# Optimization experiments

Hardware: AMD Instinct MI355X
Metric: run time of the kernel (lower is better)

## Reference

```python
import jax, jax.numpy as jnp
import numpy as np

B, T, I, H, V = 128, 80, 4096, 256, 6000
DEC_STEPS = 40


def _lstm_cell(x, h, c, Wih, Whh, b):
    # PyTorch gate order: i, f, g, o
    gates = x @ Wih.T + h @ Whh.T + b  # (B, 4H)
    i, f, g, o = jnp.split(gates, 4, axis=-1)
    c_new = jax.nn.sigmoid(f) * c + jax.nn.sigmoid(i) * jnp.tanh(g)
    h_new = jax.nn.sigmoid(o) * jnp.tanh(c_new)
    return h_new, c_new


def _lstm_scan(xs, h0, c0, Wih, Whh, b):
    # xs: (T, B, D)
    def step(carry, x):
        h, c = carry
        h, c = _lstm_cell(x, h, c, Wih, Whh, b)
        return (h, c), h
    (h, c), ys = jax.lax.scan(step, (h0, c0), xs)
    return ys, h, c


def setup_inputs() -> dict:
    key = jax.random.key(0)
    ks = jax.random.split(key, 11)
    s = 1.0 / np.sqrt(H)  # pytorch default LSTM init scale
    return {
        "x": jax.random.normal(ks[0], (B, T, I), jnp.float32),
        "W_ih1": jax.random.uniform(ks[1], (4 * H, I), jnp.float32, -s, s),
        "W_hh1": jax.random.uniform(ks[2], (4 * H, H), jnp.float32, -s, s),
        "b_ih1": jax.random.uniform(ks[3], (4 * H,), jnp.float32, -s, s),
        "b_hh1": jax.random.uniform(ks[4], (4 * H,), jnp.float32, -s, s),
        "W_ih2": jax.random.uniform(ks[5], (4 * H, H), jnp.float32, -s, s),
        "W_hh2": jax.random.uniform(ks[6], (4 * H, H), jnp.float32, -s, s),
        "b_ih2": jax.random.uniform(ks[7], (4 * H,), jnp.float32, -s, s),
        "b_ih2": jax.random.uniform(ks[7], (4 * H,), jnp.float32, -s, s),
        "b_hh2": jax.random.uniform(ks[8], (4 * H,), jnp.float32, -s, s),
        "W_out": jax.random.uniform(ks[9], (V, H), jnp.float32, -s, s),
        "b_out": jax.random.uniform(ks[10], (V,), jnp.float32, -s, s),
    }


def reference(x, W_ih1, W_hh1, b_ih1, b_hh1, W_ih2, W_hh2, b_ih2, b_hh2, W_out, b_out):
    batch = x.shape[0]
    b1 = b_ih1 + b_hh1
    b2 = b_ih2 + b_hh2
    z = jnp.zeros((batch, H), x.dtype)

    # --- Encoding: lstm1 over video features, lstm2 over lstm1 outputs ---
    xs = jnp.transpose(x, (1, 0, 2))  # (T, B, I)
    ys1, h1, c1 = _lstm_scan(xs, z, z, W_ih1, W_hh1, b1)
    _, h2, c2 = _lstm_scan(ys1, z, z, W_ih2, W_hh2, b2)

    # --- One extra lstm1 step with zero padding (as in the source) ---
    dec_pad = jnp.zeros((batch, I), x.dtype)
    h1, c1 = _lstm_cell(dec_pad, h1, c1, W_ih1, W_hh1, b1)
    y2 = jnp.zeros((batch, H), x.dtype)

    def dec_step(carry, _):
        h1, c1, h2, c2, y2 = carry
        h1, c1 = _lstm_cell(dec_pad, h1, c1, W_ih1, W_hh1, b1)
        h2, c2 = _lstm_cell(h1 + y2, h2, c2, W_ih2, W_hh2, b2)
        return (h1, c1, h2, c2, h2), h2

    _, ys = jax.lax.scan(dec_step, (h1, c1, h2, c2, y2), None, length=DEC_STEPS)  # (40, B, H)
    feats = jnp.transpose(ys, (1, 0, 2)).reshape(-1, H)  # (B*40, H)
    return feats @ W_out.T + b_out  # (B*40, V)
```

## Files before the change

### kernel.cpp

```cpp
#include <hip/hip_runtime.h>

#define NB 128
#define NT 80
#define NI 4096
#define NH 256
#define G4 1024
#define NV 6000
#define NVP 6016
#define NDEC 40

typedef unsigned short ushort_t;
typedef __attribute__((ext_vector_type(8))) short bf16x8;
typedef __attribute__((ext_vector_type(4))) float f32x4;

__device__ __forceinline__ unsigned short f2bf(float f) {
  unsigned int x = __float_as_uint(f);
  x += 0x7FFFu + ((x >> 16) & 1u);
  return (unsigned short)(x >> 16);
}
__device__ __forceinline__ ushort4 pack4(float4 v) {
  return make_ushort4(f2bf(v.x), f2bf(v.y), f2bf(v.z), f2bf(v.w));
}
__device__ __forceinline__ float ftanh(float x) {
  float xc = fminf(fmaxf(x, -12.f), 12.f);
  float e = __expf(2.f * xc);
  return (e - 1.f) * __builtin_amdgcn_rcpf(e + 1.f);
}
__device__ __forceinline__ float fsig(float x) {
  return __builtin_amdgcn_rcpf(1.f + __expf(-x));
}


__global__ __launch_bounds__(256) void k_cast_x(const float* __restrict__ x,
                                                ushort_t* __restrict__ xb) {
  const int t = blockIdx.x, b = blockIdx.y;
  const float* src = x + ((size_t)b * NT + t) * NI;
  ushort_t* dst = xb + ((size_t)t * NB + b) * NI;
#pragma unroll
  for (int s = 0; s < 4; ++s) {
    int j = s * 1024 + threadIdx.x * 4;
    float4 v = *(const float4*)(src + j);
    *(ushort4*)(dst + j) = pack4(v);
  }
}

__global__ __launch_bounds__(256) void k_cast_pad(const float* __restrict__ s,
                                                  ushort_t* __restrict__ d,
                                                  int nsrc, int ndst) {
  int i = (blockIdx.x * 256 + threadIdx.x) * 4;
  if (i >= ndst) return;
  ushort4 o;
  if (i < nsrc) {
    float4 v = *(const float4*)(s + i);
    o = pack4(v);
  } else {
    o = make_ushort4(0, 0, 0, 0);
  }
  *(ushort4*)(d + i) = o;
}

__global__ __launch_bounds__(256) void k_addw_bf(const float* __restrict__ a,
                                                 const float* __restrict__ b,
                                                 ushort_t* __restrict__ o) {
  int i = (blockIdx.x * 256 + threadIdx.x) * 4;
  float4 va = *(const float4*)(a + i);
  float4 vb = *(const float4*)(b + i);
  va.x += vb.x; va.y += vb.y; va.z += vb.z; va.w += vb.w;
  *(ushort4*)(o + i) = pack4(va);
}


#define GLDS(gp, lp)                                                     \
  __builtin_amdgcn_global_load_lds(                                      \
      (const __attribute__((address_space(1))) unsigned int*)(gp),       \
      (__attribute__((address_space(3))) unsigned int*)(lp), 16, 0, 0)

__global__ __launch_bounds__(256) void k_gemm(
    const ushort_t* __restrict__ A, const ushort_t* __restrict__ Bm,
    float* __restrict__ C, const float* __restrict__ ba,
    const float* __restrict__ bb, int Nreal, int K, int ldc, int mtiles) {
  __shared__ __align__(16) ushort_t Als[128 * 32];
  __shared__ __align__(16) ushort_t Bls[128 * 32];
  const int bid = blockIdx.x;
  const int mt = bid % mtiles, nt = bid / mtiles;
  const size_t m0 = (size_t)mt * 128, n0 = (size_t)nt * 128;
  const int tid = threadIdx.x, wave = tid >> 6, lane = tid & 63;
  const int wm = (wave & 1) * 64, wn = (wave >> 1) * 64;
  const int srow = wave * 16 + (lane >> 2), skcol = (lane & 3) * 8;
  const int fr = lane & 15, kb = (lane >> 4) * 8;

  f32x4 acc[4][4];
#pragma unroll
  for (int i = 0; i < 4; ++i)
#pragma unroll
    for (int j = 0; j < 4; ++j) acc[i][j] = (f32x4){0.f, 0.f, 0.f, 0.f};

  for (int kk = 0; kk < K; kk += 32) {
    __syncthreads();
#pragma unroll
    for (int p = 0; p < 2; ++p) {
      GLDS(A + (m0 + p * 64 + srow) * K + kk + skcol,
           &Als[(p * 64 + wave * 16) * 32]);
      GLDS(Bm + (n0 + p * 64 + srow) * K + kk + skcol,
           &Bls[(p * 64 + wave * 16) * 32]);
    }
    __syncthreads();
    bf16x8 af[4], bfr[4];
#pragma unroll
    for (int i = 0; i < 4; ++i)
      af[i] = *(const bf16x8*)&Als[(wm + i * 16 + fr) * 32 + kb];
#pragma unroll
    for (int j = 0; j < 4; ++j)
      bfr[j] = *(const bf16x8*)&Bls[(wn + j * 16 + fr) * 32 + kb];
#pragma unroll
    for (int i = 0; i < 4; ++i)
#pragma unroll
      for (int j = 0; j < 4; ++j)
        acc[i][j] = __builtin_amdgcn_mfma_f32_16x16x32_bf16(af[i], bfr[j],
                                                            acc[i][j], 0, 0, 0);
  }
  const int cr4 = (lane >> 4) * 4, ccn = lane & 15;
#pragma unroll
  for (int j = 0; j < 4; ++j) {
    int n = (int)n0 + wn + j * 16 + ccn;
    if (n < Nreal) {
      float bv = (ba ? ba[n] : 0.f) + (bb ? bb[n] : 0.f);
#pragma unroll
      for (int i = 0; i < 4; ++i) {
#pragma unroll
        for (int r = 0; r < 4; ++r) {
          size_t m = m0 + wm + i * 16 + cr4 + r;
          C[m * (size_t)ldc + n] = acc[i][j][r] + bv;
        }
      }
    }
  }
}


struct ChainArgs {
  const float* gIn0; const float* gIn1; int n0; int tStart; int tEnd;
  const ushort_t* W0; const ushort_t* Wsw; int swStep;
  const float* biasA; const float* biasB;
  ushort_t* traj0; ushort_t* traj1; int t1bmaj;
  ushort_t* hSt; float* cSt;
};

#define LOAD_WREGS(Wb)                                                        \
  _Pragma("unroll") for (int g = 0; g < 3; ++g)                               \
  _Pragma("unroll") for (int h = 0; h < 2; ++h)                               \
  _Pragma("unroll") for (int kb = 0; kb < 8; ++kb)                            \
      wr[g * 2 + h][kb] = *(const bf16x8*)((Wb) +                             \
          (size_t)(g * 256 + cbase + h * 16 + cn) * NH + kb * 32 + kgrp * 8);

#define PIN_W()                                                               \
  _Pragma("unroll") for (int g = 0; g < 6; ++g)                               \
  _Pragma("unroll") for (int kb = 0; kb < 8; ++kb)                            \
      asm volatile("" : "+a"(wr[g][kb]));

#define LOAD_WLDS(Wb)                                                         \
  _Pragma("unroll") for (int h = 0; h < 2; ++h)                               \
  _Pragma("unroll") for (int kb = 0; kb < 8; ++kb)                            \
      *(bf16x8*)&WL[wv * 8192 + h * 4096 + kb * 512 + cn * 32 + kgrp * 8] =   \
          *(const bf16x8*)((Wb) +                                             \
          (size_t)(768 + cbase + h * 16 + cn) * NH + kb * 32 + kgrp * 8);

__device__ __forceinline__ void run_chain(const ChainArgs a, int bg,
                                          ushort_t* WL,
                                          ushort_t (*hTz)[16 * 264]) {
  const int tid = threadIdx.x;
  const int wv = tid >> 6, lane = tid & 63;
  const int cn = lane & 15;
  const int kgrp = lane >> 4;
  const int cbase = wv * 32;
  const int rsel = kgrp & 1;

  bf16x8 wr[6][8];
  const ushort_t* Winit = (a.Wsw && a.tStart >= a.swStep) ? a.Wsw : a.W0;
  LOAD_WREGS(Winit);
  PIN_W();
  LOAD_WLDS(Winit);

  for (int i = tid; i < 2 * 16 * 264; i += 512) ((ushort_t*)hTz)[i] = 0;
  __syncthreads();
  float cs[8];
  if (a.tStart == 0) {
#pragma unroll
    for (int i = 0; i < 8; ++i) cs[i] = 0.f;
  } else {
    for (int i = tid; i < 8 * 256; i += 512) {
      int b = i >> 8, col = i & 255;
      hTz[0][b * 264 + col] = a.hSt[(size_t)(bg * 8 + b) * NH + col];
    }
#pragma unroll
    for (int h = 0; h < 2; ++h)
#pragma unroll
      for (int e = 0; e < 4; ++e)
        cs[h * 4 + e] =
            a.cSt[(size_t)(bg * 8 + rsel * 4 + e) * NH + cbase + h * 16 + cn];
  }
  __syncthreads();

  int cur = 0;
  for (int t = a.tStart; t < a.tEnd; ++t) {
    if (a.Wsw && t == a.swStep && t != a.tStart) {
      LOAD_WREGS(a.Wsw);
      PIN_W();
      LOAD_WLDS(a.Wsw);
      __syncthreads();
    }
    const ushort_t* hTc = &hTz[cur][0];
    ushort_t* hTn = &hTz[cur ^ 1][0];
    const float* gseg = (t < a.n0) ? a.gIn0 : a.gIn1;
    const int tt = (t < a.n0) ? t : t - a.n0;
#pragma unroll
    for (int h = 0; h < 2; ++h) {
      const int gcol = cbase + h * 16 + cn;
      float in_[4][4];
      if (gseg) {
        const float* base = gseg + (size_t)tt * (NB * G4);
#pragma unroll
        for (int g = 0; g < 4; ++g)
#pragma unroll
          for (int e = 0; e < 4; ++e)
            in_[g][e] = base[(size_t)(bg * 8 + rsel * 4 + e) * G4 + g * 256 + gcol];
      } else {
#pragma unroll
        for (int g = 0; g < 4; ++g) {
          float b = a.biasA[g * 256 + gcol] + a.biasB[g * 256 + gcol];
#pragma unroll
          for (int e = 0; e < 4; ++e) in_[g][e] = b;
        }
      }
      f32x4 acc[4];
#pragma unroll
      for (int g = 0; g < 4; ++g) acc[g] = (f32x4){0.f, 0.f, 0.f, 0.f};
#pragma unroll
      for (int kb = 0; kb < 8; ++kb) {
        bf16x8 af = *(const bf16x8*)&hTc[cn * 264 + kb * 32 + kgrp * 8];
        bf16x8 bo = *(const bf16x8*)&WL[wv * 8192 + h * 4096 + kb * 512 +
                                        cn * 32 + kgrp * 8];
        acc[0] = __builtin_amdgcn_mfma_f32_16x16x32_bf16(af, wr[0 + h][kb],
                                                         acc[0], 0, 0, 0);
        acc[1] = __builtin_amdgcn_mfma_f32_16x16x32_bf16(af, wr[2 + h][kb],
                                                         acc[1], 0, 0, 0);
        acc[2] = __builtin_amdgcn_mfma_f32_16x16x32_bf16(af, wr[4 + h][kb],
                                                         acc[2], 0, 0, 0);
        acc[3] = __builtin_amdgcn_mfma_f32_16x16x32_bf16(af, bo, acc[3], 0, 0, 0);
      }
#pragma unroll
      for (int e = 0; e < 4; ++e) {
        float a0 = acc[0][e] + in_[0][e];
        float a1 = acc[1][e] + in_[1][e];
        float a2 = acc[2][e] + in_[2][e];
        float a3 = acc[3][e] + in_[3][e];
        float ig = fsig(a0);
        float fg = fsig(a1);
        float gg = ftanh(a2);
        float og = fsig(a3);
        float cn_ = fg * cs[h * 4 + e] + ig * gg;
        cs[h * 4 + e] = cn_;
        float hn = og * ftanh(cn_);
        unsigned short hb = f2bf(hn);
        if (lane < 32) {
          const int b = (lane >> 4) * 4 + e;
          hTn[b * 264 + gcol] = hb;
          const int bglob = bg * 8 + b;
          if (t < a.n0) {
            if (a.traj0)
              a.traj0[(size_t)t * (NB * NH) + (size_t)bglob * NH + gcol] = hb;
          } else if (a.traj1) {
            size_t idx = a.t1bmaj
                ? ((size_t)bglob * NDEC + (t - a.n0)) * NH + gcol
                : (size_t)(t - a.n0) * (NB * NH) + (size_t)bglob * NH + gcol;
            a.traj1[idx] = hb;
          }
        }
      }
    }
    __syncthreads();
    cur ^= 1;
  }

  for (int i = tid; i < 8 * 256; i += 512) {
    int b = i >> 8, col = i & 255;
    a.hSt[(size_t)(bg * 8 + b) * NH + col] = hTz[cur][b * 264 + col];
  }
  if (lane < 32) {
#pragma unroll
    for (int h = 0; h < 2; ++h)
#pragma unroll
      for (int e = 0; e < 4; ++e)
        a.cSt[(size_t)(bg * 8 + (lane >> 4) * 4 + e) * NH + cbase + h * 16 + cn] =
            cs[h * 4 + e];
  }
}

__global__ __launch_bounds__(512, 1) void p_lstm16(ChainArgs a) {
  __shared__ __align__(16) ushort_t WL[8 * 8192];
  __shared__ __align__(16) ushort_t hTz[2][16 * 264];
  run_chain(a, blockIdx.x, WL, hTz);
}

__global__ __launch_bounds__(512, 1) void p_dual(ChainArgs a, ChainArgs b) {
  __shared__ __align__(16) ushort_t WL[8 * 8192];
  __shared__ __align__(16) ushort_t hTz[2][16 * 264];
  if (blockIdx.x < 16)
    run_chain(a, blockIdx.x, WL, hTz);
  else
    run_chain(b, blockIdx.x - 16, WL, hTz);
}


extern "C" void kernel_launch(void* const* d_in, const int* in_sizes, int n_in,
                              void* d_out, int out_size, void* d_ws,
                              size_t ws_size, hipStream_t stream) {
  const float* x = (const float*)d_in[0];
  const float* Wih1 = (const float*)d_in[1];
  const float* Whh1 = (const float*)d_in[2];
  const float* bih1 = (const float*)d_in[3];
  const float* bhh1 = (const float*)d_in[4];
  const float* Wih2 = (const float*)d_in[5];
  const float* Whh2 = (const float*)d_in[6];
  const float* bih2 = (const float*)d_in[7];
  const float* bhh2 = (const float*)d_in[8];
  const float* Wout = (const float*)d_in[9];
  const float* bout = (const float*)d_in[10];
  char* ws = (char*)d_ws;

  ushort_t* x_bf   = (ushort_t*)(ws + 0);
  float*    G2buf  = (float*)(ws + 0);
  float*    G3buf  = (float*)(ws + 41943040);
  float*    Gbuf   = (float*)(ws + 83886080);
  ushort_t* Wih1b  = (ushort_t*)(ws + 125829120);
  ushort_t* h1St   = (ushort_t*)(ws + 125829120);
  float*    c1St   = (float*)(ws + 125894656);
  ushort_t* h2St   = (ushort_t*)(ws + 126025728);
  float*    c2St   = (float*)(ws + 126091264);
  ushort_t* Wih2b  = (ushort_t*)(ws + 134217728);
  ushort_t* Woutb  = (ushort_t*)(ws + 134742016);
  ushort_t* Whh1b  = (ushort_t*)(ws + 137822208);
  ushort_t* Whh2b  = (ushort_t*)(ws + 138346496);
  ushort_t* ys1    = (ushort_t*)(ws + 138870784);
  ushort_t* H1dec  = (ushort_t*)(ws + 144113664);
  ushort_t* feats  = (ushort_t*)(ws + 146800640);
  ushort_t* Wsumb  = (ushort_t*)(ws + 149422080);

  k_cast_x<<<dim3(NT, NB), 256, 0, stream>>>(x, x_bf);
  k_cast_pad<<<4096, 256, 0, stream>>>(Wih1, Wih1b, G4 * NI, G4 * NI);
  k_cast_pad<<<256, 256, 0, stream>>>(Wih2, Wih2b, G4 * NH, G4 * NH);
  k_cast_pad<<<1504, 256, 0, stream>>>(Wout, Woutb, NV * NH, NVP * NH);
  k_cast_pad<<<256, 256, 0, stream>>>(Whh1, Whh1b, G4 * NH, G4 * NH);
  k_cast_pad<<<256, 256, 0, stream>>>(Whh2, Whh2b, G4 * NH, G4 * NH);
  k_addw_bf<<<256, 256, 0, stream>>>(Wih2, Whh2, Wsumb);

  k_gemm<<<640, 256, 0, stream>>>(x_bf, Wih1b, Gbuf, bih1, bhh1, G4, NI, G4, 80);

  ChainArgs c1{Gbuf, nullptr, NT, 0, 0, Whh1b, nullptr, 1 << 30,
               bih1, bhh1, ys1, H1dec, 0, h1St, c1St};
  ChainArgs c2{G2buf, G3buf, NT, 0, 0, Whh2b, Wsumb, NT + 1,
               bih2, bhh2, nullptr, feats, 1, h2St, c2St};

  ChainArgs e1a = c1; e1a.tStart = 0; e1a.tEnd = 40;
  p_lstm16<<<16, 512, 0, stream>>>(e1a);

  k_gemm<<<320, 256, 0, stream>>>(ys1, Wih2b, G2buf, bih2, bhh2, G4, NH, G4, 40);

  ChainArgs e1b = c1; e1b.tStart = 40; e1b.tEnd = 80;
  ChainArgs e2a = c2; e2a.tStart = 0; e2a.tEnd = 40;
  p_dual<<<32, 512, 0, stream>>>(e1b, e2a);

  k_gemm<<<320, 256, 0, stream>>>(ys1 + (size_t)40 * NB * NH, Wih2b,
                                  G2buf + (size_t)40 * NB * G4, bih2, bhh2,
                                  G4, NH, G4, 40);

  ChainArgs p1 = c1; p1.tStart = 80; p1.tEnd = 121;
  ChainArgs e2b = c2; e2b.tStart = 40; e2b.tEnd = 80;
  p_dual<<<32, 512, 0, stream>>>(p1, e2b);

  k_gemm<<<320, 256, 0, stream>>>(H1dec + (size_t)NB * NH, Wih2b, G3buf, bih2,
                                  bhh2, G4, NH, G4, 40);

  ChainArgs d2 = c2; d2.tStart = 80; d2.tEnd = 120;
  p_lstm16<<<16, 512, 0, stream>>>(d2);

  k_gemm<<<40 * 47, 256, 0, stream>>>(feats, Woutb, (float*)d_out, bout, nullptr,
                                      NV, NH, NV, 40);
}
```

Measured before the change: 1.332 ms.

## Fuse x bf16 cast into input GEMM and simplify decoder weight switch

Removes the separate kernel that casts and transposes x to bf16, and converts fp32 x to bf16 inside the input-projection GEMM while staging the A tile into LDS. This drops one write and one read of the large bf16 copy of x. The decoder's second-layer chain now always uses the summed weight (Wih2+Whh2) from the start, so the in-loop weight-switch path goes away. The first-step mismatch this creates is corrected by a small kernel that subtracts h2 from the first decoder h1 input. The fused GEMM loses the async global-to-LDS path for A, issuing synchronous float loads plus conversion instead, which may stall the MFMA loop.

```diff
diff --git a/kernel.cpp b/kernel.cpp
--- a/kernel.cpp
+++ b/kernel.cpp
@@ -18,6 +18,9 @@
   x += 0x7FFFu + ((x >> 16) & 1u);
   return (unsigned short)(x >> 16);
 }
+__device__ __forceinline__ float bf2f(ushort_t u) {
+  return __uint_as_float(((unsigned)u) << 16);
+}
 __device__ __forceinline__ ushort4 pack4(float4 v) {
   return make_ushort4(f2bf(v.x), f2bf(v.y), f2bf(v.z), f2bf(v.w));
 }
@@ -30,19 +33,6 @@
   return __builtin_amdgcn_rcpf(1.f + __expf(-x));
 }
 
-
-__global__ __launch_bounds__(256) void k_cast_x(const float* __restrict__ x,
-                                                ushort_t* __restrict__ xb) {
-  const int t = blockIdx.x, b = blockIdx.y;
-  const float* src = x + ((size_t)b * NT + t) * NI;
-  ushort_t* dst = xb + ((size_t)t * NB + b) * NI;
-#pragma unroll
-  for (int s = 0; s < 4; ++s) {
-    int j = s * 1024 + threadIdx.x * 4;
-    float4 v = *(const float4*)(src + j);
-    *(ushort4*)(dst + j) = pack4(v);
-  }
-}
 
 __global__ __launch_bounds__(256) void k_cast_pad(const float* __restrict__ s,
                                                   ushort_t* __restrict__ d,
@@ -67,6 +57,15 @@
   float4 vb = *(const float4*)(b + i);
   va.x += vb.x; va.y += vb.y; va.z += vb.z; va.w += vb.w;
   *(ushort4*)(o + i) = pack4(va);
+}
+
+__global__ __launch_bounds__(256) void k_subh(ushort_t* __restrict__ H1,
+                                              const ushort_t* __restrict__ h2) {
+  int i = (blockIdx.x * 256 + threadIdx.x) * 4;
+  ushort_t* p = H1 + (size_t)NB * NH + i;
+  const ushort_t* q = h2 + i;
+#pragma unroll
+  for (int k = 0; k < 4; ++k) p[k] = f2bf(bf2f(p[k]) - bf2f(q[k]));
 }
 
 
@@ -137,10 +136,76 @@
   }
 }
 
+__global__ __launch_bounds__(256) void k_gemm_xf32(
+    const float* __restrict__ X, const ushort_t* __restrict__ Bm,
+    float* __restrict__ C, const float* __restrict__ ba,
+    const float* __restrict__ bb, int mtiles) {
+  __shared__ __align__(16) ushort_t Als[128 * 40];
+  __shared__ __align__(16) ushort_t Bls[128 * 32];
+  const int bid = blockIdx.x;
+  const int mt = bid % mtiles, nt = bid / mtiles;
+  const size_t m0 = (size_t)mt * 128, n0 = (size_t)nt * 128;
+  const int tid = threadIdx.x, wave = tid >> 6, lane = tid & 63;
+  const int wm = (wave & 1) * 64, wn = (wave >> 1) * 64;
+  const int srow = wave * 16 + (lane >> 2), skcol = (lane & 3) * 8;
+  const int fr = lane & 15, kb = (lane >> 4) * 8;
+
+  f32x4 acc[4][4];
+#pragma unroll
+  for (int i = 0; i < 4; ++i)
+#pragma unroll
+    for (int j = 0; j < 4; ++j) acc[i][j] = (f32x4){0.f, 0.f, 0.f, 0.f};
+
+  for (int kk = 0; kk < NI; kk += 32) {
+    __syncthreads();
+#pragma unroll
+    for (int p = 0; p < 2; ++p)
+      GLDS(Bm + (n0 + p * 64 + srow) * NI + kk + skcol,
+           &Bls[(p * 64 + wave * 16) * 32]);
+#pragma unroll
+    for (int p = 0; p < 2; ++p) {
+      int r = p * 64 + srow;
+      const float* sp = X + ((size_t)r * NT + mt) * NI + kk + skcol;
+      float4 v0 = *(const float4*)sp;
+      float4 v1 = *(const float4*)(sp + 4);
+      *(ushort4*)&Als[r * 40 + skcol] = pack4(v0);
+      *(ushort4*)&Als[r * 40 + skcol + 4] = pack4(v1);
+    }
+    __syncthreads();
+    bf16x8 af[4], bfr[4];
+#pragma unroll
+    for (int i = 0; i < 4; ++i)
+      af[i] = *(const bf16x8*)&Als[(wm + i * 16 + fr) * 40 + kb];
+#pragma unroll
+    for (int j = 0; j < 4; ++j)
+      bfr[j] = *(const bf16x8*)&Bls[(wn + j * 16 + fr) * 32 + kb];
+#pragma unroll
+    for (int i = 0; i < 4; ++i)
+#pragma unroll
+      for (int j = 0; j < 4; ++j)
+        acc[i][j] = __builtin_amdgcn_mfma_f32_16x16x32_bf16(af[i], bfr[j],
+                                                            acc[i][j], 0, 0, 0);
+  }
+  const int cr4 = (lane >> 4) * 4, ccn = lane & 15;
+#pragma unroll
+  for (int j = 0; j < 4; ++j) {
+    int n = (int)n0 + wn + j * 16 + ccn;
+    float bv = ba[n] + bb[n];
+#pragma unroll
+    for (int i = 0; i < 4; ++i) {
+#pragma unroll
+      for (int r = 0; r < 4; ++r) {
+        size_t m = m0 + wm + i * 16 + cr4 + r;
+        C[m * (size_t)G4 + n] = acc[i][j][r] + bv;
+      }
+    }
+  }
+}
+
 
 struct ChainArgs {
   const float* gIn0; const float* gIn1; int n0; int tStart; int tEnd;
-  const ushort_t* W0; const ushort_t* Wsw; int swStep;
+  const ushort_t* W0;
   const float* biasA; const float* biasB;
   ushort_t* traj0; ushort_t* traj1; int t1bmaj;
   ushort_t* hSt; float* cSt;
@@ -176,10 +241,9 @@
   const int rsel = kgrp & 1;
 
   bf16x8 wr[6][8];
-  const ushort_t* Winit = (a.Wsw && a.tStart >= a.swStep) ? a.Wsw : a.W0;
-  LOAD_WREGS(Winit);
+  LOAD_WREGS(a.W0);
   PIN_W();
-  LOAD_WLDS(Winit);
+  LOAD_WLDS(a.W0);
 
   for (int i = tid; i < 2 * 16 * 264; i += 512) ((ushort_t*)hTz)[i] = 0;
   __syncthreads();
@@ -203,12 +267,6 @@
 
   int cur = 0;
   for (int t = a.tStart; t < a.tEnd; ++t) {
-    if (a.Wsw && t == a.swStep && t != a.tStart) {
-      LOAD_WREGS(a.Wsw);
-      PIN_W();
-      LOAD_WLDS(a.Wsw);
-      __syncthreads();
-    }
     const ushort_t* hTc = &hTz[cur][0];
     ushort_t* hTn = &hTz[cur ^ 1][0];
     const float* gseg = (t < a.n0) ? a.gIn0 : a.gIn1;
@@ -328,15 +386,10 @@
   const float* bout = (const float*)d_in[10];
   char* ws = (char*)d_ws;
 
-  ushort_t* x_bf   = (ushort_t*)(ws + 0);
   float*    G2buf  = (float*)(ws + 0);
   float*    G3buf  = (float*)(ws + 41943040);
   float*    Gbuf   = (float*)(ws + 83886080);
   ushort_t* Wih1b  = (ushort_t*)(ws + 125829120);
-  ushort_t* h1St   = (ushort_t*)(ws + 125829120);
-  float*    c1St   = (float*)(ws + 125894656);
-  ushort_t* h2St   = (ushort_t*)(ws + 126025728);
-  float*    c2St   = (float*)(ws + 126091264);
   ushort_t* Wih2b  = (ushort_t*)(ws + 134217728);
   ushort_t* Woutb  = (ushort_t*)(ws + 134742016);
   ushort_t* Whh1b  = (ushort_t*)(ws + 137822208);
@@ -345,8 +398,11 @@
   ushort_t* H1dec  = (ushort_t*)(ws + 144113664);
   ushort_t* feats  = (ushort_t*)(ws + 146800640);
   ushort_t* Wsumb  = (ushort_t*)(ws + 149422080);
-
-  k_cast_x<<<dim3(NT, NB), 256, 0, stream>>>(x, x_bf);
+  ushort_t* h1St   = (ushort_t*)(ws + 149946368);
+  float*    c1St   = (float*)(ws + 150011904);
+  ushort_t* h2St   = (ushort_t*)(ws + 150142976);
+  float*    c2St   = (float*)(ws + 150208512);
+
   k_cast_pad<<<4096, 256, 0, stream>>>(Wih1, Wih1b, G4 * NI, G4 * NI);
   k_cast_pad<<<256, 256, 0, stream>>>(Wih2, Wih2b, G4 * NH, G4 * NH);
   k_cast_pad<<<1504, 256, 0, stream>>>(Wout, Woutb, NV * NH, NVP * NH);
@@ -354,11 +410,11 @@
   k_cast_pad<<<256, 256, 0, stream>>>(Whh2, Whh2b, G4 * NH, G4 * NH);
   k_addw_bf<<<256, 256, 0, stream>>>(Wih2, Whh2, Wsumb);
 
-  k_gemm<<<640, 256, 0, stream>>>(x_bf, Wih1b, Gbuf, bih1, bhh1, G4, NI, G4, 80);
-
-  ChainArgs c1{Gbuf, nullptr, NT, 0, 0, Whh1b, nullptr, 1 << 30,
+  k_gemm_xf32<<<640, 256, 0, stream>>>(x, Wih1b, Gbuf, bih1, bhh1, 80);
+
+  ChainArgs c1{Gbuf, nullptr, NT, 0, 0, Whh1b,
                bih1, bhh1, ys1, H1dec, 0, h1St, c1St};
-  ChainArgs c2{G2buf, G3buf, NT, 0, 0, Whh2b, Wsumb, NT + 1,
+  ChainArgs c2{G2buf, G3buf, NT, 0, 0, Whh2b,
                bih2, bhh2, nullptr, feats, 1, h2St, c2St};
 
   ChainArgs e1a = c1; e1a.tStart = 0; e1a.tEnd = 40;
@@ -378,10 +434,12 @@
   ChainArgs e2b = c2; e2b.tStart = 40; e2b.tEnd = 80;
   p_dual<<<32, 512, 0, stream>>>(p1, e2b);
 
+  k_subh<<<32, 256, 0, stream>>>(H1dec, h2St);
+
   k_gemm<<<320, 256, 0, stream>>>(H1dec + (size_t)NB * NH, Wih2b, G3buf, bih2,
                                   bhh2, G4, NH, G4, 40);
 
-  ChainArgs d2 = c2; d2.tStart = 80; d2.tEnd = 120;
+  ChainArgs d2 = c2; d2.W0 = Wsumb; d2.tStart = 80; d2.tEnd = 120;
   p_lstm16<<<16, 512, 0, stream>>>(d2);
 
   k_gemm<<<40 * 47, 256, 0, stream>>>(feats, Woutb, (float*)d_out, bout, nullptr,
```

Measured after the change: 1.341 ms. About the same (+0.7%).
